# Optimization experiments

Measured on AMD Instinct MI355X. Metric: run time of the kernel, lower is better.

The kernel has to match this reference:

```python
import jax, jax.numpy as jnp
import numpy as np

B, C, K, H, W = 8, 64, 32, 128, 128  # K = num_cluster // 2
NEG_SLOPE = 0.1


def setup_inputs() -> dict:
    key = jax.random.key(0)
    k1, k2, k3, k4, k5, k6 = jax.random.split(key, 6)
    HR = jax.random.normal(k1, (B, C, H, W), jnp.float32)
    LR = jax.random.normal(k2, (B, C, H, W), jnp.float32)
    # Conv2d(1+K, 1, 1) weights flattened to [1+K] + bias, Conv2d(1,1,1) -> scalar w/b
    w1 = jax.random.normal(k3, (K + 1,), jnp.float32) * 0.1
    b1 = jax.random.normal(k4, (1,), jnp.float32) * 0.1
    w2 = jax.random.normal(k5, (1,), jnp.float32) * 0.1
    b2 = jax.random.normal(k6, (1,), jnp.float32) * 0.1
    return {"HR": HR, "LR": LR, "w1": w1, "b1": b1, "w2": w2, "b2": b2}


def reference(HR, LR, w1, b1, w2, b2):
    Bn, Cn = HR.shape[0], HR.shape[1]
    HRf = HR.reshape(Bn, Cn, -1)                      # [B, C, HW]
    LRf = LR.reshape(Bn, Cn, -1)                      # [B, C, HW]
    corr = jnp.einsum('bcn,bdn->bcd', LRf, HRf)       # [B, C_lr, C_hr]
    _, idx = jax.lax.top_k(corr, K)                   # [B, C, K] (int32)
    # gather top-K HR channels per LR channel: [B, C, K, H, W]
    gathered = jax.vmap(lambda h, ix: h[ix])(HR, idx)
    weight = jax.nn.sigmoid(jnp.max(gathered, axis=2))        # [B, C, H, W]
    # 1x1 conv over the (1+K) concatenated channels == weighted sum
    fusion = w1[0] * LR + jnp.einsum('bckhw,k->bchw', gathered, w1[1:]) + b1[0]
    fusion = jnp.where(fusion >= 0, fusion, NEG_SLOPE * fusion)  # LeakyReLU(0.1)
    fusion = w2[0] * fusion + b2[0]                   # second 1x1 conv
    return fusion * (1.0 + weight)                    # fusion + weight*fusion
```

## Files before the change

kernel.cpp:

```cpp
#include <hip/hip_runtime.h>
#include <math.h>

#define B_ 8
#define C_ 64
#define K_ 32
#define HW_ 16384
#define CHUNK_ 128
#define NCHUNKOUT_ 64
#define LDN 132
#define TILE_ 256
#define NEG_SLOPE_ 0.1f


__global__ __launch_bounds__(256, 2) void corr_partial_kernel(
    const float* __restrict__ LR, const float* __restrict__ HR,
    float* __restrict__ partial)
{
    __shared__ float lrS[C_][LDN];
    __shared__ float hrS[C_][LDN];
    const int blk = blockIdx.x;
    const int b = blk >> 6;
    const int j = blk & 63;
    const int t = threadIdx.x;

    const int cq = t >> 4;
    const int dq = t & 15;
    float acc[4][4] = {};

    for (int half = 0; half < 2; ++half) {
        const int n0 = (j * 2 + half) * CHUNK_;
        if (half) __syncthreads();
        #pragma unroll
        for (int p = 0; p < 8; ++p) {
            const int f = p * 256 + t;
            const int c = f >> 5;
            const int q = f & 31;
            *reinterpret_cast<float4*>(&lrS[c][q * 4]) =
                *reinterpret_cast<const float4*>(&LR[(size_t)(b * C_ + c) * HW_ + n0 + q * 4]);
            *reinterpret_cast<float4*>(&hrS[c][q * 4]) =
                *reinterpret_cast<const float4*>(&HR[(size_t)(b * C_ + c) * HW_ + n0 + q * 4]);
        }
        __syncthreads();

        for (int nq = 0; nq < 32; ++nq) {
            float4 lv[4], hv[4];
            #pragma unroll
            for (int i = 0; i < 4; ++i)
                lv[i] = *reinterpret_cast<const float4*>(&lrS[cq + 16 * i][nq * 4]);
            #pragma unroll
            for (int jj = 0; jj < 4; ++jj)
                hv[jj] = *reinterpret_cast<const float4*>(&hrS[dq + 16 * jj][nq * 4]);
            #pragma unroll
            for (int i = 0; i < 4; ++i) {
                const float l[4] = {lv[i].x, lv[i].y, lv[i].z, lv[i].w};
                #pragma unroll
                for (int jj = 0; jj < 4; ++jj) {
                    const float h[4] = {hv[jj].x, hv[jj].y, hv[jj].z, hv[jj].w};
                    acc[i][jj] = fmaf(l[0], h[0], acc[i][jj]);
                    acc[i][jj] = fmaf(l[1], h[1], acc[i][jj]);
                    acc[i][jj] = fmaf(l[2], h[2], acc[i][jj]);
                    acc[i][jj] = fmaf(l[3], h[3], acc[i][jj]);
                }
            }
        }
    }

    float* P = partial + (size_t)(b * NCHUNKOUT_ + j) * (C_ * C_);
    #pragma unroll
    for (int i = 0; i < 4; ++i)
        #pragma unroll
        for (int jj = 0; jj < 4; ++jj)
            P[(cq + 16 * i) * C_ + (dq + 16 * jj)] = acc[i][jj];
}

__global__ __launch_bounds__(64) void rank_kernel(
    const float* __restrict__ partial, int* __restrict__ idxb)
{
    __shared__ double vals[C_];
    const int blk = blockIdx.x;
    const int b = blk >> 6;
    const int c = blk & 63;
    const int d = threadIdx.x;

    double acc = 0.0;
    for (int k = 0; k < NCHUNKOUT_; ++k)
        acc += (double)partial[(size_t)(b * NCHUNKOUT_ + k) * (C_ * C_) + c * C_ + d];
    vals[d] = acc;
    __syncthreads();

    int r = 0;
    for (int jj = 0; jj < C_; ++jj) {
        const double vj = vals[jj];
        r += (int)((vj > acc) || (vj == acc && jj < d));
    }
    if (r < K_) idxb[blk * K_ + r] = d;
}

__global__ __launch_bounds__(256, 2) void fusion_gather_kernel(
    const float* __restrict__ HR, const float* __restrict__ LR,
    const int* __restrict__ idxb,
    const float* __restrict__ w1, const float* __restrict__ b1,
    const float* __restrict__ w2, const float* __restrict__ b2,
    float* __restrict__ out)
{
    __shared__ float hrS[C_][TILE_];

    const int t = threadIdx.x;
    const int bid = blockIdx.x;
    const int b = bid >> 6;
    const int px0 = (bid & 63) * TILE_;

    const float* HRb = HR + (size_t)b * C_ * HW_;
    #pragma unroll
    for (int i = 0; i < 16; ++i) {
        const int f = i * 256 + t;
        const int c = f >> 6;
        const int q = f & 63;
        *reinterpret_cast<float4*>(&hrS[c][q * 4]) =
            *reinterpret_cast<const float4*>(&HRb[(size_t)c * HW_ + px0 + q * 4]);
    }
    __syncthreads();

    const int wv = t >> 6;
    const int lane = t & 63;
    const int p4 = lane * 4;

    const int* idxc = idxb + b * C_ * K_;
    const float w10 = w1[0];
    const float b1v = b1[0], w2v = w2[0], b2v = b2[0];

    #pragma unroll 1
    for (int ci = 0; ci < 16; ++ci) {
        const int c = wv * 16 + ci;
        const float4 l4 = *reinterpret_cast<const float4*>(
            &LR[(size_t)(b * C_ + c) * HW_ + px0 + p4]);
        float acc[4] = {0.f, 0.f, 0.f, 0.f};
        float mx[4]  = {-1e30f, -1e30f, -1e30f, -1e30f};
        #pragma unroll
        for (int k = 0; k < K_; ++k) {
            const int d = idxc[c * K_ + k];
            const float4 h = *reinterpret_cast<const float4*>(&hrS[d][p4]);
            const float wk = w1[k + 1];
            acc[0] = fmaf(h.x, wk, acc[0]);
            acc[1] = fmaf(h.y, wk, acc[1]);
            acc[2] = fmaf(h.z, wk, acc[2]);
            acc[3] = fmaf(h.w, wk, acc[3]);
            mx[0] = fmaxf(mx[0], h.x);
            mx[1] = fmaxf(mx[1], h.y);
            mx[2] = fmaxf(mx[2], h.z);
            mx[3] = fmaxf(mx[3], h.w);
        }
        const float l[4] = {l4.x, l4.y, l4.z, l4.w};
        float o[4];
        #pragma unroll
        for (int p = 0; p < 4; ++p) {
            float f = fmaf(w10, l[p], acc[p]) + b1v;
            f = f >= 0.f ? f : NEG_SLOPE_ * f;
            f = fmaf(w2v, f, b2v);
            const float s = 1.f / (1.f + __expf(-mx[p]));
            o[p] = f * (1.f + s);
        }
        *reinterpret_cast<float4*>(&out[(size_t)(b * C_ + c) * HW_ + px0 + p4]) =
            make_float4(o[0], o[1], o[2], o[3]);
    }
}

extern "C" void kernel_launch(void* const* d_in, const int* in_sizes, int n_in,
                              void* d_out, int out_size, void* d_ws, size_t ws_size,
                              hipStream_t stream)
{
    const float* HR = (const float*)d_in[0];
    const float* LR = (const float*)d_in[1];
    const float* w1 = (const float*)d_in[2];
    const float* b1 = (const float*)d_in[3];
    const float* w2 = (const float*)d_in[4];
    const float* b2 = (const float*)d_in[5];
    float* out = (float*)d_out;

    float* partial = (float*)d_ws;
    int* idxb = (int*)((char*)d_ws + (size_t)B_ * NCHUNKOUT_ * C_ * C_ * sizeof(float));

    corr_partial_kernel<<<B_ * NCHUNKOUT_, 256, 0, stream>>>(LR, HR, partial);
    rank_kernel<<<B_ * C_, 64, 0, stream>>>(partial, idxb);
    fusion_gather_kernel<<<B_ * (HW_ / TILE_), 256, 0, stream>>>(HR, LR, idxb, w1, b1, w2, b2, out);
}
```

Before: 59.79 us.

## Give each wavefront its own 64x64 correlation tile and parallelize partial reduction

The correlation kernel now has each wavefront compute a full 64x64 outer-product accumulator (8x8 per lane) over its own 32-pixel slices, with per-wave shared-memory staging and no block-wide barriers. This produces four times as many partial matrices. The rank kernel uses 256 threads to reduce them in four groups before ranking. The trade is more register pressure (64 accumulators per lane) and more partial traffic to write and read, in exchange for removing the syncthreads stalls and getting more register reuse per shared load.

```diff
diff --git a/kernel.cpp b/kernel.cpp
--- a/kernel.cpp
+++ b/kernel.cpp
@@ -5,9 +5,8 @@
 #define C_ 64
 #define K_ 32
 #define HW_ 16384
-#define CHUNK_ 128
-#define NCHUNKOUT_ 64
-#define LDN 132
+#define SROW 36
+#define NPART_ 256
 #define TILE_ 256
 #define NEG_SLOPE_ 0.1f
 
@@ -16,84 +15,92 @@
     const float* __restrict__ LR, const float* __restrict__ HR,
     float* __restrict__ partial)
 {
-    __shared__ float lrS[C_][LDN];
-    __shared__ float hrS[C_][LDN];
-    const int blk = blockIdx.x;
-    const int b = blk >> 6;
-    const int j = blk & 63;
+    __shared__ float lrS[4][C_][SROW];
+    __shared__ float hrS[4][C_][SROW];
+    const int bid = blockIdx.x;
+    const int b = bid >> 6;
+    const int q = bid & 63;
     const int t = threadIdx.x;
+    const int wv = t >> 6;
+    const int lane = t & 63;
+    const int cq = lane >> 3;
+    const int dq = lane & 7;
 
-    const int cq = t >> 4;
-    const int dq = t & 15;
-    float acc[4][4] = {};
+    float acc[8][8] = {};
 
-    for (int half = 0; half < 2; ++half) {
-        const int n0 = (j * 2 + half) * CHUNK_;
-        if (half) __syncthreads();
+    #pragma unroll 1
+    for (int s = 0; s < 2; ++s) {
+        const int n0 = (((q * 4 + wv) << 1) + s) * 32;
         #pragma unroll
-        for (int p = 0; p < 8; ++p) {
-            const int f = p * 256 + t;
-            const int c = f >> 5;
-            const int q = f & 31;
-            *reinterpret_cast<float4*>(&lrS[c][q * 4]) =
-                *reinterpret_cast<const float4*>(&LR[(size_t)(b * C_ + c) * HW_ + n0 + q * 4]);
-            *reinterpret_cast<float4*>(&hrS[c][q * 4]) =
-                *reinterpret_cast<const float4*>(&HR[(size_t)(b * C_ + c) * HW_ + n0 + q * 4]);
+        for (int i = 0; i < 8; ++i) {
+            const int c = i * 8 + (lane >> 3);
+            const int col = (lane & 7) * 4;
+            *reinterpret_cast<float4*>(&lrS[wv][c][col]) =
+                *reinterpret_cast<const float4*>(&LR[(size_t)(b * C_ + c) * HW_ + n0 + col]);
+            *reinterpret_cast<float4*>(&hrS[wv][c][col]) =
+                *reinterpret_cast<const float4*>(&HR[(size_t)(b * C_ + c) * HW_ + n0 + col]);
         }
-        __syncthreads();
-
-        for (int nq = 0; nq < 32; ++nq) {
-            float4 lv[4], hv[4];
+        #pragma unroll 2
+        for (int nq = 0; nq < 8; ++nq) {
+            float4 lv[8], hv[8];
             #pragma unroll
-            for (int i = 0; i < 4; ++i)
-                lv[i] = *reinterpret_cast<const float4*>(&lrS[cq + 16 * i][nq * 4]);
+            for (int i = 0; i < 8; ++i)
+                lv[i] = *reinterpret_cast<const float4*>(&lrS[wv][cq + 8 * i][nq * 4]);
             #pragma unroll
-            for (int jj = 0; jj < 4; ++jj)
-                hv[jj] = *reinterpret_cast<const float4*>(&hrS[dq + 16 * jj][nq * 4]);
+            for (int j = 0; j < 8; ++j)
+                hv[j] = *reinterpret_cast<const float4*>(&hrS[wv][dq + 8 * j][nq * 4]);
             #pragma unroll
-            for (int i = 0; i < 4; ++i) {
-                const float l[4] = {lv[i].x, lv[i].y, lv[i].z, lv[i].w};
+            for (int i = 0; i < 8; ++i)
                 #pragma unroll
-                for (int jj = 0; jj < 4; ++jj) {
-                    const float h[4] = {hv[jj].x, hv[jj].y, hv[jj].z, hv[jj].w};
-                    acc[i][jj] = fmaf(l[0], h[0], acc[i][jj]);
-                    acc[i][jj] = fmaf(l[1], h[1], acc[i][jj]);
-                    acc[i][jj] = fmaf(l[2], h[2], acc[i][jj]);
-                    acc[i][jj] = fmaf(l[3], h[3], acc[i][jj]);
+                for (int j = 0; j < 8; ++j) {
+                    acc[i][j] = fmaf(lv[i].x, hv[j].x, acc[i][j]);
+                    acc[i][j] = fmaf(lv[i].y, hv[j].y, acc[i][j]);
+                    acc[i][j] = fmaf(lv[i].z, hv[j].z, acc[i][j]);
+                    acc[i][j] = fmaf(lv[i].w, hv[j].w, acc[i][j]);
                 }
-            }
         }
     }
 
-    float* P = partial + (size_t)(b * NCHUNKOUT_ + j) * (C_ * C_);
+    const int pid = q * 4 + wv;
+    float* P = partial + (size_t)(b * NPART_ + pid) * (C_ * C_);
     #pragma unroll
-    for (int i = 0; i < 4; ++i)
+    for (int i = 0; i < 8; ++i)
         #pragma unroll
-        for (int jj = 0; jj < 4; ++jj)
-            P[(cq + 16 * i) * C_ + (dq + 16 * jj)] = acc[i][jj];
+        for (int j = 0; j < 8; ++j)
+            P[(cq + 8 * i) * C_ + (dq + 8 * j)] = acc[i][j];
 }
 
-__global__ __launch_bounds__(64) void rank_kernel(
+__global__ __launch_bounds__(256) void rank_kernel(
     const float* __restrict__ partial, int* __restrict__ idxb)
 {
+    __shared__ double sh[4][C_];
     __shared__ double vals[C_];
     const int blk = blockIdx.x;
     const int b = blk >> 6;
     const int c = blk & 63;
-    const int d = threadIdx.x;
+    const int g = threadIdx.x >> 6;
+    const int d = threadIdx.x & 63;
 
     double acc = 0.0;
-    for (int k = 0; k < NCHUNKOUT_; ++k)
-        acc += (double)partial[(size_t)(b * NCHUNKOUT_ + k) * (C_ * C_) + c * C_ + d];
-    vals[d] = acc;
+    for (int k = 0; k < 64; ++k)
+        acc += (double)partial[(size_t)(b * NPART_ + g * 64 + k) * (C_ * C_) + c * C_ + d];
+    sh[g][d] = acc;
     __syncthreads();
 
-    int r = 0;
-    for (int jj = 0; jj < C_; ++jj) {
-        const double vj = vals[jj];
-        r += (int)((vj > acc) || (vj == acc && jj < d));
+    if (threadIdx.x < 64) {
+        vals[d] = ((sh[0][d] + sh[1][d]) + sh[2][d]) + sh[3][d];
     }
-    if (r < K_) idxb[blk * K_ + r] = d;
+    __syncthreads();
+
+    if (threadIdx.x < 64) {
+        const double vd = vals[d];
+        int r = 0;
+        for (int j = 0; j < C_; ++j) {
+            const double vj = vals[j];
+            r += (int)((vj > vd) || (vj == vd && j < d));
+        }
+        if (r < K_) idxb[blk * K_ + r] = d;
+    }
 }
 
 __global__ __launch_bounds__(256, 2) void fusion_gather_kernel(
@@ -178,9 +185,9 @@
     float* out = (float*)d_out;
 
     float* partial = (float*)d_ws;
-    int* idxb = (int*)((char*)d_ws + (size_t)B_ * NCHUNKOUT_ * C_ * C_ * sizeof(float));
+    int* idxb = (int*)((char*)d_ws + (size_t)B_ * NPART_ * C_ * C_ * sizeof(float));
 
-    corr_partial_kernel<<<B_ * NCHUNKOUT_, 256, 0, stream>>>(LR, HR, partial);
-    rank_kernel<<<B_ * C_, 64, 0, stream>>>(partial, idxb);
+    corr_partial_kernel<<<B_ * 64, 256, 0, stream>>>(LR, HR, partial);
+    rank_kernel<<<B_ * C_, 256, 0, stream>>>(partial, idxb);
     fusion_gather_kernel<<<B_ * (HW_ / TILE_), 256, 0, stream>>>(HR, LR, idxb, w1, b1, w2, b2, out);
 }
```

Measured after the change: 66.30 us. +10.9%, slower.

## Double-buffer HR tile prefetch in fusion kernel with 512-thread blocks

Applied to the files above, without the earlier changes.

The fusion kernel now uses 512-thread blocks that each process two consecutive 256-pixel tiles. While computing the first tile, the block prefetches the second tile's HR data into registers. The aim is to hide global-load latency behind the gather compute and to cut per-channel work per wave. The trade-off is half as many blocks (256 on a large GPU), more register pressure from the prefetch buffers, and an extra barrier.

```diff
diff --git a/kernel.cpp b/kernel.cpp
--- a/kernel.cpp
+++ b/kernel.cpp
@@ -96,7 +96,7 @@
     if (r < K_) idxb[blk * K_ + r] = d;
 }
 
-__global__ __launch_bounds__(256, 2) void fusion_gather_kernel(
+__global__ __launch_bounds__(512, 1) void fusion_gather_kernel(
     const float* __restrict__ HR, const float* __restrict__ LR,
     const int* __restrict__ idxb,
     const float* __restrict__ w1, const float* __restrict__ b1,
@@ -107,19 +107,25 @@
 
     const int t = threadIdx.x;
     const int bid = blockIdx.x;
-    const int b = bid >> 6;
-    const int px0 = (bid & 63) * TILE_;
-
+    const int g0 = bid * 2;
+    const int b = g0 >> 6;
     const float* HRb = HR + (size_t)b * C_ * HW_;
+
+    int sc[8], sq[8];
     #pragma unroll
-    for (int i = 0; i < 16; ++i) {
-        const int f = i * 256 + t;
-        const int c = f >> 6;
-        const int q = f & 63;
-        *reinterpret_cast<float4*>(&hrS[c][q * 4]) =
-            *reinterpret_cast<const float4*>(&HRb[(size_t)c * HW_ + px0 + q * 4]);
-    }
-    __syncthreads();
+    for (int i = 0; i < 8; ++i) {
+        const int f = i * 512 + t;
+        sc[i] = f >> 6;
+        sq[i] = (f & 63) * 4;
+    }
+
+    float4 pre[8];
+    {
+        const int px0 = (g0 & 63) * TILE_;
+        #pragma unroll
+        for (int i = 0; i < 8; ++i)
+            pre[i] = *reinterpret_cast<const float4*>(&HRb[(size_t)sc[i] * HW_ + px0 + sq[i]]);
+    }
 
     const int wv = t >> 6;
     const int lane = t & 63;
@@ -130,38 +136,55 @@
     const float b1v = b1[0], w2v = w2[0], b2v = b2[0];
 
     #pragma unroll 1
-    for (int ci = 0; ci < 16; ++ci) {
-        const int c = wv * 16 + ci;
-        const float4 l4 = *reinterpret_cast<const float4*>(
-            &LR[(size_t)(b * C_ + c) * HW_ + px0 + p4]);
-        float acc[4] = {0.f, 0.f, 0.f, 0.f};
-        float mx[4]  = {-1e30f, -1e30f, -1e30f, -1e30f};
-        #pragma unroll
-        for (int k = 0; k < K_; ++k) {
-            const int d = idxc[c * K_ + k];
-            const float4 h = *reinterpret_cast<const float4*>(&hrS[d][p4]);
-            const float wk = w1[k + 1];
-            acc[0] = fmaf(h.x, wk, acc[0]);
-            acc[1] = fmaf(h.y, wk, acc[1]);
-            acc[2] = fmaf(h.z, wk, acc[2]);
-            acc[3] = fmaf(h.w, wk, acc[3]);
-            mx[0] = fmaxf(mx[0], h.x);
-            mx[1] = fmaxf(mx[1], h.y);
-            mx[2] = fmaxf(mx[2], h.z);
-            mx[3] = fmaxf(mx[3], h.w);
-        }
-        const float l[4] = {l4.x, l4.y, l4.z, l4.w};
-        float o[4];
-        #pragma unroll
-        for (int p = 0; p < 4; ++p) {
-            float f = fmaf(w10, l[p], acc[p]) + b1v;
-            f = f >= 0.f ? f : NEG_SLOPE_ * f;
-            f = fmaf(w2v, f, b2v);
-            const float s = 1.f / (1.f + __expf(-mx[p]));
-            o[p] = f * (1.f + s);
-        }
-        *reinterpret_cast<float4*>(&out[(size_t)(b * C_ + c) * HW_ + px0 + p4]) =
-            make_float4(o[0], o[1], o[2], o[3]);
+    for (int it = 0; it < 2; ++it) {
+        const int px0 = ((g0 + it) & 63) * TILE_;
+        if (it) __syncthreads();
+        #pragma unroll
+        for (int i = 0; i < 8; ++i)
+            *reinterpret_cast<float4*>(&hrS[sc[i]][sq[i]]) = pre[i];
+        __syncthreads();
+
+        if (it == 0) {
+            const int px1 = ((g0 + 1) & 63) * TILE_;
+            #pragma unroll
+            for (int i = 0; i < 8; ++i)
+                pre[i] = *reinterpret_cast<const float4*>(&HRb[(size_t)sc[i] * HW_ + px1 + sq[i]]);
+        }
+
+        #pragma unroll 1
+        for (int ci = 0; ci < 8; ++ci) {
+            const int c = wv * 8 + ci;
+            const float4 l4 = *reinterpret_cast<const float4*>(
+                &LR[(size_t)(b * C_ + c) * HW_ + px0 + p4]);
+            float acc[4] = {0.f, 0.f, 0.f, 0.f};
+            float mx[4]  = {-1e30f, -1e30f, -1e30f, -1e30f};
+            #pragma unroll
+            for (int k = 0; k < K_; ++k) {
+                const int d = idxc[c * K_ + k];
+                const float4 h = *reinterpret_cast<const float4*>(&hrS[d][p4]);
+                const float wk = w1[k + 1];
+                acc[0] = fmaf(h.x, wk, acc[0]);
+                acc[1] = fmaf(h.y, wk, acc[1]);
+                acc[2] = fmaf(h.z, wk, acc[2]);
+                acc[3] = fmaf(h.w, wk, acc[3]);
+                mx[0] = fmaxf(mx[0], h.x);
+                mx[1] = fmaxf(mx[1], h.y);
+                mx[2] = fmaxf(mx[2], h.z);
+                mx[3] = fmaxf(mx[3], h.w);
+            }
+            const float l[4] = {l4.x, l4.y, l4.z, l4.w};
+            float o[4];
+            #pragma unroll
+            for (int p = 0; p < 4; ++p) {
+                float f = fmaf(w10, l[p], acc[p]) + b1v;
+                f = f >= 0.f ? f : NEG_SLOPE_ * f;
+                f = fmaf(w2v, f, b2v);
+                const float s = 1.f / (1.f + __expf(-mx[p]));
+                o[p] = f * (1.f + s);
+            }
+            *reinterpret_cast<float4*>(&out[(size_t)(b * C_ + c) * HW_ + px0 + p4]) =
+                make_float4(o[0], o[1], o[2], o[3]);
+        }
     }
 }
 
@@ -180,7 +203,7 @@
     float* partial = (float*)d_ws;
     int* idxb = (int*)((char*)d_ws + (size_t)B_ * NCHUNKOUT_ * C_ * C_ * sizeof(float));
 
-    corr_partial_kernel<<<B_ * NCHUNKOUT_, 256, 0, stream>>>(LR, HR, partial);
+    corr_partial_kernel<<<B_ * 64, 256, 0, stream>>>(LR, HR, partial);
     rank_kernel<<<B_ * C_, 64, 0, stream>>>(partial, idxb);
-    fusion_gather_kernel<<<B_ * (HW_ / TILE_), 256, 0, stream>>>(HR, LR, idxb, w1, b1, w2, b2, out);
-}
+    fusion_gather_kernel<<<B_ * (HW_ / TILE_) / 2, 512, 0, stream>>>(HR, LR, idxb, w1, b1, w2, b2, out);
+}
```

New measurement: 73.58 us. +23.0%, slower.
